# Optimization experiments

Measured on AMD Instinct MI355X. Metric: run time of the kernel, lower is better.

The kernel has to match this reference:

```python
import jax, jax.numpy as jnp
import numpy as np


def setup_inputs() -> dict:
    key = jax.random.key(0)
    k1, k2, k3 = jax.random.split(key, 3)
    B, T, D = 2, 2048, 1024
    x = jax.random.normal(k1, (B, T, D), dtype=jnp.float32)
    w_qkv = jax.random.normal(k2, (3 * D, D), dtype=jnp.float32) * (D ** -0.5)
    w_out = jax.random.normal(k3, (D, D), dtype=jnp.float32) * (D ** -0.5)
    return {"x": x, "w_qkv": w_qkv, "w_out": w_out, "heads": 16}


def reference(x, w_qkv, w_out, heads):
    # SelfAttention forward: attention_type='sdp', position_mode='alibi', causal=True, eval mode.
    B, T, D = x.shape
    H = heads
    hd = D // H
    scale = hd ** -0.5

    # qkv projection: torch Linear -> x @ W^T
    qkv = (x @ w_qkv.T).reshape(B, T, 3, H, hd)
    qkv = jnp.transpose(qkv, (2, 0, 3, 1, 4))  # [3, B, H, T, hd]
    q, k, v = qkv[0], qkv[1], qkv[2]

    # ALiBi relative bias: slopes = 1 / 2^(h/H) for h = 1..H
    slopes = 1.0 / jnp.power(2.0, jnp.arange(1, H + 1, dtype=jnp.float32) / H)
    pos = jnp.arange(T, dtype=jnp.float32)
    rel = jnp.abs(pos[:, None] - pos[None, :])  # [T, T]
    bias = -slopes[None, :, None, None] * rel[None, None, :, :]  # [1, H, T, T]

    # scores + causal mask + softmax (manual path since position_bias is not None)
    scores = jnp.einsum('bhqd,bhkd->bhqk', q, k) * scale + bias
    causal_mask = jnp.triu(jnp.ones((T, T), dtype=bool), k=1)
    scores = jnp.where(causal_mask[None, None, :, :], -jnp.inf, scores)
    attn = jax.nn.softmax(scores, axis=-1)
    attn = jnp.where(jnp.isnan(attn), 1.0 / float(max(T, 1)), attn)

    out = jnp.einsum('bhqk,bhkd->bhqd', attn, v)  # [B, H, T, hd]
    out = jnp.transpose(out, (0, 2, 1, 3)).reshape(B, T, D)
    return out @ w_out.T
```

## Files before the change

### kernel.cpp

```cpp
#include <hip/hip_runtime.h>
#include <hip/hip_bf16.h>

typedef __attribute__((ext_vector_type(8))) short shortx8;
typedef __attribute__((ext_vector_type(4))) float floatx4;
typedef __attribute__((ext_vector_type(16))) float floatx16;
typedef __attribute__((ext_vector_type(4))) unsigned uintx4;
typedef __attribute__((ext_vector_type(2))) unsigned uintx2;

#define B_ 2
#define T_ 2048
#define D_ 1024
#define H_ 16
#define HD_ 64
#define SCALE 0.125f
#define QSCALE 0.18033688011112042f
#define SMAX2 23.083120654223414f
#define FULLH ((size_t)B_ * H_ * T_ * HD_)

#define GLDS16(g, l) __builtin_amdgcn_global_load_lds( \
    (__attribute__((address_space(1))) void*)(g), \
    (__attribute__((address_space(3))) void*)(l), 16, 0, 0)

__device__ __forceinline__ short f2bf(float f) {
    union { float f; unsigned u; } v; v.f = f;
    unsigned r = v.u + 0x7FFFu + ((v.u >> 16) & 1u);
    return (short)(r >> 16);
}

__device__ __forceinline__ unsigned pk2(float x, float y) {
    union { __hip_bfloat162 h; unsigned u; } t;
    t.h = __float22bfloat162_rn(make_float2(x, y));
    return t.u;
}

__device__ __forceinline__ shortx8 cvt8(floatx4 a, floatx4 b) {
    uintx4 r = { pk2(a[0], a[1]), pk2(a[2], a[3]), pk2(b[0], b[1]), pk2(b[2], b[3]) };
    return __builtin_bit_cast(shortx8, r);
}

__device__ __forceinline__ float ex2(float x) {
#if __has_builtin(__builtin_amdgcn_exp2f)
    return __builtin_amdgcn_exp2f(x);
#else
    return exp2f(x);
#endif
}

__global__ __launch_bounds__(256) void cvt_xw(const float* __restrict__ x,
                                              const float* __restrict__ wqkv,
                                              short* __restrict__ xbf,
                                              short* __restrict__ wbf) {
    int i = blockIdx.x * 256 + threadIdx.x;
    const float* src; short* dst; int o;
    if (i < 524288) { src = x; dst = xbf; o = i; }
    else            { src = wqkv; dst = wbf; o = i - 524288; }
    const floatx4* p = reinterpret_cast<const floatx4*>(src) + (size_t)o * 2;
    *(reinterpret_cast<shortx8*>(dst) + o) = cvt8(p[0], p[1]);
}

__global__ __launch_bounds__(256) void qkv_fast(const short* __restrict__ xbf,
                                                const short* __restrict__ wbf,
                                                short* __restrict__ qout,
                                                short* __restrict__ kv) {
    __shared__ __align__(16) short As[128 * 64];
    __shared__ __align__(16) short Bs[128 * 64];

    const int tid = threadIdx.x;
    const int wv = tid >> 6;
    const int l  = tid & 63;
    const int ln = l & 15;
    const int quad = l >> 4;
    const int rowb = quad << 2;
    const int wm = wv >> 1, wn = wv & 1;

    const int id  = blockIdx.x;
    const int xcd = id & 7;
    const int tt  = id >> 3;
    const int bx  = xcd * 3 + (tt >> 5);
    const int by  = tt & 31;
    const int m0 = by * 128;
    const int n0g = bx * 128;

    const int lr = l >> 3, lc = l & 7;
    const int gcol = (lc ^ lr) << 3;
    const short* agp = xbf + (size_t)(m0 + wv * 32 + lr) * D_ + gcol;
    const short* bgp = wbf + (size_t)(n0g + wv * 32 + lr) * D_ + gcol;
    short* aldsb = As + wv * 32 * 64;
    short* bldsb = Bs + wv * 32 * 64;

    floatx4 acc[4][4] = {};

    for (int k0 = 0; k0 < D_; k0 += 64) {
        __syncthreads();
#pragma unroll
        for (int c = 0; c < 4; ++c) {
            GLDS16(agp + (size_t)(c * 8) * D_ + k0, aldsb + c * 512);
            GLDS16(bgp + (size_t)(c * 8) * D_ + k0, bldsb + c * 512);
        }
        __syncthreads();

#pragma unroll
        for (int kk = 0; kk < 2; ++kk) {
            const int csw = (kk << 2) + quad;
            const int sw = (csw ^ (ln & 7)) << 3;
            shortx8 af[4], bf[4];
#pragma unroll
            for (int i = 0; i < 4; ++i)
                af[i] = *reinterpret_cast<const shortx8*>(&As[((wm * 64 + i * 16 + ln) << 6) + sw]);
#pragma unroll
            for (int j = 0; j < 4; ++j)
                bf[j] = *reinterpret_cast<const shortx8*>(&Bs[((wn * 64 + j * 16 + ln) << 6) + sw]);
#pragma unroll
            for (int i = 0; i < 4; ++i)
#pragma unroll
                for (int j = 0; j < 4; ++j)
                    acc[i][j] = __builtin_amdgcn_mfma_f32_16x16x32_bf16(af[i], bf[j], acc[i][j], 0, 0, 0);
        }
    }

    const int sel = n0g >> 10;
    const int bb = m0 >> 11;
    const int t0w = (m0 + wm * 64) & (T_ - 1);
    const int h = ((n0g + wn * 64) >> 6) & 15;

    if (sel < 2) {
        short* dst = (sel == 0) ? qout : kv;
        const float sc = (sel == 0) ? QSCALE : 1.0f;
        const size_t hb = (size_t)(bb * H_ + h) * T_;
#pragma unroll
        for (int i = 0; i < 4; ++i)
#pragma unroll
            for (int r = 0; r < 4; ++r) {
                int t = t0w + i * 16 + rowb + r;
#pragma unroll
                for (int j = 0; j < 4; ++j)
                    dst[(hb + t) * HD_ + j * 16 + ln] = f2bf(acc[i][j][r] * sc);
            }
    } else {
        __syncthreads();
        short* tb = (wv < 2) ? (As + wv * 4096) : (Bs + (wv - 2) * 4096);
        short* vhead = kv + FULLH + (size_t)(bb * H_ + h) * HD_ * T_;
        const int dl = l & 31, th = (l >> 5) << 5;
#pragma unroll
        for (int p = 0; p < 2; ++p) {
#pragma unroll
            for (int i = 0; i < 4; ++i)
#pragma unroll
                for (int jj = 0; jj < 2; ++jj) {
                    int j = 2 * p + jj;
#pragma unroll
                    for (int r = 0; r < 4; ++r)
                        tb[(jj * 16 + ln) * 72 + i * 16 + rowb + r] = f2bf(acc[i][j][r]);
                }
            short* vd = vhead + (size_t)(p * 32 + dl) * T_ + t0w + th;
#pragma unroll
            for (int seg = 0; seg < 4; ++seg)
                *reinterpret_cast<shortx8*>(vd + seg * 8) =
                    *reinterpret_cast<const shortx8*>(&tb[dl * 72 + th + seg * 8]);
        }
    }
}

__global__ __launch_bounds__(256) void out_fast(const short* __restrict__ Abf,
                                                const short* __restrict__ wbf,
                                                float* __restrict__ out) {
    __shared__ __align__(16) short As[64 * 64];
    __shared__ __align__(16) short Bs[128 * 64];

    const int tid = threadIdx.x;
    const int wv = tid >> 6;
    const int l  = tid & 63;
    const int ln = l & 15;
    const int quad = l >> 4;
    const int rowb = quad << 2;
    const int wm = wv >> 1, wn = wv & 1;

    const int id = blockIdx.x;
    const int m0 = (id >> 3) * 64;
    const int n0g = (id & 7) * 128;

    const int lr = l >> 3, lc = l & 7;
    const int gcol = (lc ^ lr) << 3;
    const short* bgp = wbf + (size_t)(n0g + wv * 32 + lr) * D_ + gcol;
    short* aldsb = As + wv * 16 * 64;
    short* bldsb = Bs + wv * 32 * 64;

    size_t abase[2];
#pragma unroll
    for (int c = 0; c < 2; ++c) {
        int m = m0 + wv * 16 + c * 8 + lr;
        int bb2 = m >> 11, t = m & (T_ - 1);
        abase[c] = ((size_t)(bb2 * H_) * T_ + t) * HD_ + gcol;
    }

    floatx4 acc[2][4] = {};

    for (int k0 = 0; k0 < D_; k0 += 64) {
        const size_t hoff = (size_t)(k0 >> 6) * T_ * HD_;
        __syncthreads();
#pragma unroll
        for (int c = 0; c < 2; ++c)
            GLDS16(Abf + abase[c] + hoff, aldsb + c * 512);
#pragma unroll
        for (int c = 0; c < 4; ++c)
            GLDS16(bgp + (size_t)(c * 8) * D_ + k0, bldsb + c * 512);
        __syncthreads();

#pragma unroll
        for (int kk = 0; kk < 2; ++kk) {
            const int csw = (kk << 2) + quad;
            const int sw = (csw ^ (ln & 7)) << 3;
            shortx8 af[2], bf[4];
#pragma unroll
            for (int i = 0; i < 2; ++i)
                af[i] = *reinterpret_cast<const shortx8*>(&As[((wm * 32 + i * 16 + ln) << 6) + sw]);
#pragma unroll
            for (int j = 0; j < 4; ++j)
                bf[j] = *reinterpret_cast<const shortx8*>(&Bs[((wn * 64 + j * 16 + ln) << 6) + sw]);
#pragma unroll
            for (int i = 0; i < 2; ++i)
#pragma unroll
                for (int j = 0; j < 4; ++j)
                    acc[i][j] = __builtin_amdgcn_mfma_f32_16x16x32_bf16(af[i], bf[j], acc[i][j], 0, 0, 0);
        }
    }

#pragma unroll
    for (int i = 0; i < 2; ++i)
#pragma unroll
        for (int r = 0; r < 4; ++r) {
            int m = m0 + wm * 32 + i * 16 + rowb + r;
#pragma unroll
            for (int j = 0; j < 4; ++j)
                out[(size_t)m * D_ + n0g + wn * 64 + j * 16 + ln] = acc[i][j][r];
        }
}

__global__ __launch_bounds__(128, 2) void attn(const short* __restrict__ qws,
                                               const short* __restrict__ kv,
                                               short* ao,
                                               const float* __restrict__ wout,
                                               short* __restrict__ wobf) {
    if (blockIdx.x >= 1024) {
        int i = (blockIdx.x - 1024) * 128 + threadIdx.x;
        const floatx4* p = reinterpret_cast<const floatx4*>(wout) + (size_t)i * 2;
        *(reinterpret_cast<shortx8*>(wobf) + i) = cvt8(p[0], p[1]);
        return;
    }

    __shared__ __align__(16) short Ks[2][64][72];
    __shared__ __align__(16) short Vt[2][64][72];

    const int tid = threadIdx.x;
    const int wv = tid >> 6;
    const int l  = tid & 63;
    const int ql = l & 31;
    const int hi = l >> 5;

    const int id  = blockIdx.x;
    const int xcd = id & 7;
    const int u2  = (id >> 3) & 3;
    const int rr  = (id >> 5) & 7;
    const int tt  = id >> 8;
    const int bh  = xcd * 4 + u2;
    const int qblk = (tt == 0) ? 31 - rr : (tt == 1) ? rr : (tt == 2) ? 23 - rr : 8 + rr;
    const int h = bh & 15, b = bh >> 4;

    const float slope2 = 1.4426950408889634f * exp2f(-(float)(h + 1) * 0.0625f);
    const size_t koff = (size_t)(b * H_ + h) * T_ * HD_;
    const int q0w = qblk * 64 + wv * 32;
    const int e = qblk + 1;

    shortx8 qf[4];
#pragma unroll
    for (int ds = 0; ds < 4; ++ds)
        qf[ds] = *reinterpret_cast<const shortx8*>(&qws[koff + (size_t)(q0w + ql) * HD_ + ds * 16 + hi * 8]);

    const float cbase = slope2 * (float)(4 * hi - (q0w + ql)) - SMAX2;
    float rb[16];
#pragma unroll
    for (int g = 0; g < 16; ++g)
        rb[g] = cbase + slope2 * (float)((g & 3) + 8 * (g >> 2));
    const float s32 = slope2 * 32.0f;

    const int sr = tid >> 1;
    const int sc = (tid & 1) << 5;
    const short* kbase = kv + koff;
    const short* vbase = kv + FULLH + koff;
    shortx8 kR[4], vR[4];
    auto FETCH = [&](int kb) {
        const short* kp = kbase + (((size_t)(kb * 64 + sr)) << 6) + sc;
        const short* vp = vbase + (size_t)sr * T_ + kb * 64 + sc;
#pragma unroll
        for (int s = 0; s < 4; ++s) {
            kR[s] = *reinterpret_cast<const shortx8*>(kp + 8 * s);
            vR[s] = *reinterpret_cast<const shortx8*>(vp + 8 * s);
        }
    };
    auto STAGE = [&](int bi) {
#pragma unroll
        for (int s = 0; s < 4; ++s) {
            *reinterpret_cast<shortx8*>(&Ks[bi][sr][sc + 8 * s]) = kR[s];
            *reinterpret_cast<shortx8*>(&Vt[bi][sr][sc + 8 * s]) = vR[s];
        }
    };

    floatx16 o0 = {}, o1 = {}, ls = {};
    const shortx8 ones = {16256, 16256, 16256, 16256, 16256, 16256, 16256, 16256};
    const int qlh = ql - 4 * hi;

    FETCH(0);
    STAGE(0);
    if (e > 1) FETCH(1);
    __syncthreads();

    for (int kb = 0; kb < e; ++kb) {
        const int cur = kb & 1;
        if (kb + 1 < e) {
            STAGE(cur ^ 1);
            if (kb + 2 < e) FETCH(kb + 2);
        }

        const bool diag = (kb == qblk);
        const float tb = slope2 * (float)(kb * 64);

#pragma unroll
        for (int nc = 0; nc < 2; ++nc) {
            const bool act = !diag || (nc == 0) || (wv == 1);
            if (!act) continue;
            const bool part = diag && (nc == wv);

            floatx16 sacc = {};
#pragma unroll
            for (int ds = 0; ds < 4; ++ds) {
                shortx8 kf = *reinterpret_cast<const shortx8*>(&Ks[cur][nc * 32 + ql][ds * 16 + hi * 8]);
                sacc = __builtin_amdgcn_mfma_f32_32x32x16_bf16(kf, qf[ds], sacc, 0, 0, 0);
            }

            const float tnc = tb + (nc ? s32 : 0.0f);
            float p[16];
#pragma unroll
            for (int g = 0; g < 16; ++g) {
                float ev = ex2(sacc[g] + (rb[g] + tnc));
                if (part) {
                    const int kc2 = (g & 3) + 8 * (g >> 2);
                    ev = (kc2 <= qlh) ? ev : 0.0f;
                }
                p[g] = ev;
            }

            unsigned cv[4][2];
#pragma unroll
            for (int g = 0; g < 4; ++g) {
                cv[g][0] = pk2(p[4 * g + 0], p[4 * g + 1]);
                cv[g][1] = pk2(p[4 * g + 2], p[4 * g + 3]);
            }

            __builtin_amdgcn_s_setprio(1);
#pragma unroll
            for (int kh = 0; kh < 2; ++kh) {
                unsigned w0 = cv[2 * kh][0], w2 = cv[2 * kh + 1][0];
                unsigned w1 = cv[2 * kh][1], w3 = cv[2 * kh + 1][1];
                asm volatile("v_permlane32_swap_b32 %0, %1" : "+v"(w0), "+v"(w2));
                asm volatile("v_permlane32_swap_b32 %0, %1" : "+v"(w1), "+v"(w3));
                uintx4 uu = {w0, w1, w2, w3};
                shortx8 apv = __builtin_bit_cast(shortx8, uu);
                const int ks = nc * 2 + kh;
                ls = __builtin_amdgcn_mfma_f32_32x32x16_bf16(apv, ones, ls, 0, 0, 0);
                shortx8 vf0 = *reinterpret_cast<const shortx8*>(&Vt[cur][ql][ks * 16 + hi * 8]);
                o0 = __builtin_amdgcn_mfma_f32_32x32x16_bf16(apv, vf0, o0, 0, 0, 0);
                shortx8 vf1 = *reinterpret_cast<const shortx8*>(&Vt[cur][32 + ql][ks * 16 + hi * 8]);
                o1 = __builtin_amdgcn_mfma_f32_32x32x16_bf16(apv, vf1, o1, 0, 0, 0);
            }
            __builtin_amdgcn_s_setprio(0);
        }
        __syncthreads();
    }

#pragma unroll
    for (int g = 0; g < 16; ++g) {
        const int qrow = (g & 3) + 8 * (g >> 2) + 4 * hi;
        const float inv = 1.0f / ls[g];
        const size_t ob = koff + (size_t)(q0w + qrow) * HD_ + ql;
        ao[ob]      = f2bf(o0[g] * inv);
        ao[ob + 32] = f2bf(o1[g] * inv);
    }
}

__global__ __launch_bounds__(256) void qkv_slow(const float* __restrict__ x,
                                                const float* __restrict__ wqkv,
                                                short* __restrict__ qout,
                                                short* __restrict__ kv) {
    __shared__ __align__(16) short As[64][72];
    __shared__ __align__(16) short Bs[64][72];
    const int tid = threadIdx.x;
    const int wv = tid >> 6, l = tid & 63, ln = l & 15, quad = l >> 4, qd = quad << 3;
    const int m0 = blockIdx.y * 64;
    const int sel = blockIdx.x >> 4, h = blockIdx.x & 15;
    const int nrow = sel * D_ + h * HD_;
    const int sr0 = tid >> 3, sc0 = (tid & 7) << 3, sr1 = sr0 + 32;
    floatx4 fa[4], fb[4];
    auto FETCH = [&](int k0) {
        const float* ap = &x[(size_t)(m0 + sr0) * D_ + k0 + sc0];
        fa[0] = *reinterpret_cast<const floatx4*>(ap);
        fa[1] = *reinterpret_cast<const floatx4*>(ap + 4);
        ap += (size_t)32 * D_;
        fa[2] = *reinterpret_cast<const floatx4*>(ap);
        fa[3] = *reinterpret_cast<const floatx4*>(ap + 4);
        const float* bp = &wqkv[(size_t)(nrow + sr0) * D_ + k0 + sc0];
        fb[0] = *reinterpret_cast<const floatx4*>(bp);
        fb[1] = *reinterpret_cast<const floatx4*>(bp + 4);
        bp += (size_t)32 * D_;
        fb[2] = *reinterpret_cast<const floatx4*>(bp);
        fb[3] = *reinterpret_cast<const floatx4*>(bp + 4);
    };
    floatx4 acc[4] = {};
    FETCH(0);
    for (int k0 = 0; k0 < D_; k0 += 64) {
        __syncthreads();
        *reinterpret_cast<shortx8*>(&As[sr0][sc0]) = cvt8(fa[0], fa[1]);
        *reinterpret_cast<shortx8*>(&As[sr1][sc0]) = cvt8(fa[2], fa[3]);
        *reinterpret_cast<shortx8*>(&Bs[sr0][sc0]) = cvt8(fb[0], fb[1]);
        *reinterpret_cast<shortx8*>(&Bs[sr1][sc0]) = cvt8(fb[2], fb[3]);
        __syncthreads();
        if (k0 + 64 < D_) FETCH(k0 + 64);
        const int mr = (wv << 4) + ln;
#pragma unroll
        for (int kk = 0; kk < 2; ++kk) {
            shortx8 a = *reinterpret_cast<const shortx8*>(&As[mr][kk * 32 + qd]);
#pragma unroll
            for (int nc = 0; nc < 4; ++nc) {
                shortx8 bq = *reinterpret_cast<const shortx8*>(&Bs[nc * 16 + ln][kk * 32 + qd]);
                acc[nc] = __builtin_amdgcn_mfma_f32_16x16x32_bf16(a, bq, acc[nc], 0, 0, 0);
            }
        }
    }
    const int bb = m0 >> 11, t0 = m0 & (T_ - 1);
    if (sel < 2) {
        short* dst = (sel == 0) ? qout : kv;
        const float sc = (sel == 0) ? QSCALE : 1.0f;
#pragma unroll
        for (int r = 0; r < 4; ++r) {
            int t = t0 + (wv << 4) + (quad << 2) + r;
#pragma unroll
            for (int nc = 0; nc < 4; ++nc)
                dst[((size_t)(bb * H_ + h) * T_ + t) * HD_ + nc * 16 + ln] = f2bf(acc[nc][r] * sc);
        }
    } else {
        __syncthreads();
#pragma unroll
        for (int r = 0; r < 4; ++r)
#pragma unroll
            for (int nc = 0; nc < 4; ++nc)
                As[nc * 16 + ln][(wv << 4) + (quad << 2) + r] = f2bf(acc[nc][r]);
        __syncthreads();
        const int d = tid >> 2, tseg = (tid & 3) << 4;
        short* vdst = kv + FULLH + ((size_t)(bb * H_ + h) * HD_ + d) * T_ + t0 + tseg;
        *reinterpret_cast<shortx8*>(vdst)     = *reinterpret_cast<const shortx8*>(&As[d][tseg]);
        *reinterpret_cast<shortx8*>(vdst + 8) = *reinterpret_cast<const shortx8*>(&As[d][tseg + 8]);
    }
}

__global__ __launch_bounds__(256) void out_slow(const short* __restrict__ A,
                                                const float* __restrict__ W,
                                                float* __restrict__ out) {
    __shared__ __align__(16) short As[64][72];
    __shared__ __align__(16) short Bs[64][72];
    const int tid = threadIdx.x;
    const int wv = tid >> 6, l = tid & 63, ln = l & 15, quad = l >> 4, qd = quad << 3;
    const int m0 = blockIdx.y * 64, n0 = blockIdx.x * 64;
    const int sr0 = tid >> 3, sc0 = (tid & 7) << 3, sr1 = sr0 + 32;
    shortx8 sa0, sa1;
    floatx4 fb[4];
    auto FETCH = [&](int k0) {
        const int h = k0 >> 6;
        int m = m0 + sr0;
        int bb = m >> 11, t = m & (T_ - 1);
        sa0 = *reinterpret_cast<const shortx8*>(A + ((size_t)(bb * H_ + h) * T_ + t) * HD_ + sc0);
        m = m0 + sr1; bb = m >> 11; t = m & (T_ - 1);
        sa1 = *reinterpret_cast<const shortx8*>(A + ((size_t)(bb * H_ + h) * T_ + t) * HD_ + sc0);
        const float* bp = &W[(size_t)(n0 + sr0) * D_ + k0 + sc0];
        fb[0] = *reinterpret_cast<const floatx4*>(bp);
        fb[1] = *reinterpret_cast<const floatx4*>(bp + 4);
        bp += (size_t)32 * D_;
        fb[2] = *reinterpret_cast<const floatx4*>(bp);
        fb[3] = *reinterpret_cast<const floatx4*>(bp + 4);
    };
    floatx4 acc[4] = {};
    FETCH(0);
    for (int k0 = 0; k0 < D_; k0 += 64) {
        __syncthreads();
        *reinterpret_cast<shortx8*>(&As[sr0][sc0]) = sa0;
        *reinterpret_cast<shortx8*>(&As[sr1][sc0]) = sa1;
        *reinterpret_cast<shortx8*>(&Bs[sr0][sc0]) = cvt8(fb[0], fb[1]);
        *reinterpret_cast<shortx8*>(&Bs[sr1][sc0]) = cvt8(fb[2], fb[3]);
        __syncthreads();
        if (k0 + 64 < D_) FETCH(k0 + 64);
        const int mr = (wv << 4) + ln;
#pragma unroll
        for (int kk = 0; kk < 2; ++kk) {
            shortx8 a = *reinterpret_cast<const shortx8*>(&As[mr][kk * 32 + qd]);
#pragma unroll
            for (int nc = 0; nc < 4; ++nc) {
                shortx8 bq = *reinterpret_cast<const shortx8*>(&Bs[nc * 16 + ln][kk * 32 + qd]);
                acc[nc] = __builtin_amdgcn_mfma_f32_16x16x32_bf16(a, bq, acc[nc], 0, 0, 0);
            }
        }
    }
#pragma unroll
    for (int r = 0; r < 4; ++r) {
        int m = m0 + (wv << 4) + (quad << 2) + r;
#pragma unroll
        for (int nc = 0; nc < 4; ++nc)
            out[(size_t)m * D_ + n0 + nc * 16 + ln] = acc[nc][r];
    }
}

extern "C" void kernel_launch(void* const* d_in, const int* in_sizes, int n_in,
                              void* d_out, int out_size, void* d_ws, size_t ws_size,
                              hipStream_t stream) {
    const float* x    = (const float*)d_in[0];
    const float* wqkv = (const float*)d_in[1];
    const float* wout = (const float*)d_in[2];

    short* kvbuf = (short*)d_out;
    float* out   = (float*)d_out;

    if (ws_size >= 23068672ULL) {
        short* xbf  = (short*)d_ws;
        short* wbf  = xbf + 4 * 1024 * 1024;
        short* qws  = xbf + 7 * 1024 * 1024;
        short* wobf = xbf;

        cvt_xw<<<3584, 256, 0, stream>>>(x, wqkv, xbf, wbf);
        qkv_fast<<<dim3(768), 256, 0, stream>>>(xbf, wbf, qws, kvbuf);
        attn<<<dim3(2048), 128, 0, stream>>>(qws, kvbuf, qws, wout, wobf);
        out_fast<<<dim3(512), 256, 0, stream>>>(qws, wobf, out);
    } else {
        short* qws = (short*)d_ws;
        qkv_slow<<<dim3(48, 64), 256, 0, stream>>>(x, wqkv, qws, kvbuf);
        attn<<<dim3(1024), 128, 0, stream>>>(qws, kvbuf, qws, nullptr, nullptr);
        out_slow<<<dim3(16, 64), 256, 0, stream>>>(qws, wout, out);
    }
}
```

Before: 181.4 us.

## Double-buffer LDS tiles in QKV and output GEMMs and remap QKV block order

Both projection GEMMs now use two LDS buffers per operand. The next K-tile is prefetched with global_load_lds while the current tile feeds the MFMAs, which removes one barrier per iteration and hides global load latency. The QKV kernel also changes its block-to-tile mapping so that groups of 8 row tiles are walked per column group within each XCD, aiming for better L2 reuse. The cost is doubled LDS per block, which may lower occupancy, and the compiler may insert conservative waits that limit the overlap.

```diff
diff --git a/kernel.cpp b/kernel.cpp
--- a/kernel.cpp
+++ b/kernel.cpp
@@ -62,8 +62,8 @@
                                                 const short* __restrict__ wbf,
                                                 short* __restrict__ qout,
                                                 short* __restrict__ kv) {
-    __shared__ __align__(16) short As[128 * 64];
-    __shared__ __align__(16) short Bs[128 * 64];
+    __shared__ __align__(16) short As[2][128 * 64];
+    __shared__ __align__(16) short Bs[2][128 * 64];
 
     const int tid = threadIdx.x;
     const int wv = tid >> 6;
@@ -76,8 +76,12 @@
     const int id  = blockIdx.x;
     const int xcd = id & 7;
     const int tt  = id >> 3;
-    const int bx  = xcd * 3 + (tt >> 5);
-    const int by  = tt & 31;
+    const int byi = tt & 7;
+    const int u   = tt >> 3;
+    const int bxl = u % 3;
+    const int chunk = u / 3;
+    const int bx = xcd * 3 + bxl;
+    const int by = chunk * 8 + byi;
     const int m0 = by * 128;
     const int n0g = bx * 128;
 
@@ -85,19 +89,26 @@
     const int gcol = (lc ^ lr) << 3;
     const short* agp = xbf + (size_t)(m0 + wv * 32 + lr) * D_ + gcol;
     const short* bgp = wbf + (size_t)(n0g + wv * 32 + lr) * D_ + gcol;
-    short* aldsb = As + wv * 32 * 64;
-    short* bldsb = Bs + wv * 32 * 64;
 
     floatx4 acc[4][4] = {};
 
-    for (int k0 = 0; k0 < D_; k0 += 64) {
-        __syncthreads();
-#pragma unroll
-        for (int c = 0; c < 4; ++c) {
-            GLDS16(agp + (size_t)(c * 8) * D_ + k0, aldsb + c * 512);
-            GLDS16(bgp + (size_t)(c * 8) * D_ + k0, bldsb + c * 512);
-        }
-        __syncthreads();
+#pragma unroll
+    for (int c = 0; c < 4; ++c) {
+        GLDS16(agp + (size_t)(c * 8) * D_, &As[0][wv * 2048 + c * 512]);
+        GLDS16(bgp + (size_t)(c * 8) * D_, &Bs[0][wv * 2048 + c * 512]);
+    }
+
+    for (int it = 0; it < 16; ++it) {
+        const int cur = it & 1;
+        __syncthreads();
+        if (it < 15) {
+            const size_t k0n = (size_t)(it + 1) * 64;
+#pragma unroll
+            for (int c = 0; c < 4; ++c) {
+                GLDS16(agp + (size_t)(c * 8) * D_ + k0n, &As[cur ^ 1][wv * 2048 + c * 512]);
+                GLDS16(bgp + (size_t)(c * 8) * D_ + k0n, &Bs[cur ^ 1][wv * 2048 + c * 512]);
+            }
+        }
 
 #pragma unroll
         for (int kk = 0; kk < 2; ++kk) {
@@ -106,10 +117,10 @@
             shortx8 af[4], bf[4];
 #pragma unroll
             for (int i = 0; i < 4; ++i)
-                af[i] = *reinterpret_cast<const shortx8*>(&As[((wm * 64 + i * 16 + ln) << 6) + sw]);
+                af[i] = *reinterpret_cast<const shortx8*>(&As[cur][((wm * 64 + i * 16 + ln) << 6) + sw]);
 #pragma unroll
             for (int j = 0; j < 4; ++j)
-                bf[j] = *reinterpret_cast<const shortx8*>(&Bs[((wn * 64 + j * 16 + ln) << 6) + sw]);
+                bf[j] = *reinterpret_cast<const shortx8*>(&Bs[cur][((wn * 64 + j * 16 + ln) << 6) + sw]);
 #pragma unroll
             for (int i = 0; i < 4; ++i)
 #pragma unroll
@@ -138,7 +149,7 @@
             }
     } else {
         __syncthreads();
-        short* tb = (wv < 2) ? (As + wv * 4096) : (Bs + (wv - 2) * 4096);
+        short* tb = &As[0][0] + wv * 4096;
         short* vhead = kv + FULLH + (size_t)(bb * H_ + h) * HD_ * T_;
         const int dl = l & 31, th = (l >> 5) << 5;
 #pragma unroll
@@ -164,8 +175,8 @@
 __global__ __launch_bounds__(256) void out_fast(const short* __restrict__ Abf,
                                                 const short* __restrict__ wbf,
                                                 float* __restrict__ out) {
-    __shared__ __align__(16) short As[64 * 64];
-    __shared__ __align__(16) short Bs[128 * 64];
+    __shared__ __align__(16) short As[2][64 * 64];
+    __shared__ __align__(16) short Bs[2][128 * 64];
 
     const int tid = threadIdx.x;
     const int wv = tid >> 6;
@@ -182,8 +193,6 @@
     const int lr = l >> 3, lc = l & 7;
     const int gcol = (lc ^ lr) << 3;
     const short* bgp = wbf + (size_t)(n0g + wv * 32 + lr) * D_ + gcol;
-    short* aldsb = As + wv * 16 * 64;
-    short* bldsb = Bs + wv * 32 * 64;
 
     size_t abase[2];
 #pragma unroll
@@ -195,16 +204,26 @@
 
     floatx4 acc[2][4] = {};
 
-    for (int k0 = 0; k0 < D_; k0 += 64) {
-        const size_t hoff = (size_t)(k0 >> 6) * T_ * HD_;
-        __syncthreads();
-#pragma unroll
-        for (int c = 0; c < 2; ++c)
-            GLDS16(Abf + abase[c] + hoff, aldsb + c * 512);
-#pragma unroll
-        for (int c = 0; c < 4; ++c)
-            GLDS16(bgp + (size_t)(c * 8) * D_ + k0, bldsb + c * 512);
-        __syncthreads();
+#pragma unroll
+    for (int c = 0; c < 2; ++c)
+        GLDS16(Abf + abase[c], &As[0][wv * 1024 + c * 512]);
+#pragma unroll
+    for (int c = 0; c < 4; ++c)
+        GLDS16(bgp + (size_t)(c * 8) * D_, &Bs[0][wv * 2048 + c * 512]);
+
+    for (int it = 0; it < 16; ++it) {
+        const int cur = it & 1;
+        __syncthreads();
+        if (it < 15) {
+            const size_t hoffn = (size_t)(it + 1) * T_ * HD_;
+            const size_t k0n = (size_t)(it + 1) * 64;
+#pragma unroll
+            for (int c = 0; c < 2; ++c)
+                GLDS16(Abf + abase[c] + hoffn, &As[cur ^ 1][wv * 1024 + c * 512]);
+#pragma unroll
+            for (int c = 0; c < 4; ++c)
+                GLDS16(bgp + (size_t)(c * 8) * D_ + k0n, &Bs[cur ^ 1][wv * 2048 + c * 512]);
+        }
 
 #pragma unroll
         for (int kk = 0; kk < 2; ++kk) {
@@ -213,10 +232,10 @@
             shortx8 af[2], bf[4];
 #pragma unroll
             for (int i = 0; i < 2; ++i)
-                af[i] = *reinterpret_cast<const shortx8*>(&As[((wm * 32 + i * 16 + ln) << 6) + sw]);
+                af[i] = *reinterpret_cast<const shortx8*>(&As[cur][((wm * 32 + i * 16 + ln) << 6) + sw]);
 #pragma unroll
             for (int j = 0; j < 4; ++j)
-                bf[j] = *reinterpret_cast<const shortx8*>(&Bs[((wn * 64 + j * 16 + ln) << 6) + sw]);
+                bf[j] = *reinterpret_cast<const shortx8*>(&Bs[cur][((wn * 64 + j * 16 + ln) << 6) + sw]);
 #pragma unroll
             for (int i = 0; i < 2; ++i)
 #pragma unroll
```

Result: slower. 185.2 us (+2.1%).

## Fuse fp32-to-bf16 conversion into QKV GEMM with register-prefetched staging

Applied to the files above, without the earlier changes.

Removes the separate cvt_xw kernel and has the QKV GEMM load fp32 x and w_qkv directly, converting to bf16 in registers and writing padded LDS tiles. The next k-tile is prefetched into registers while MFMAs run, replacing the async global_load_lds path. This saves one launch and a bf16 round trip through global memory, but doubles the bytes each GEMM block reads from global memory and adds register pressure. The block-to-tile mapping is also reordered for L2 locality.

```diff
diff --git a/kernel.cpp b/kernel.cpp
--- a/kernel.cpp
+++ b/kernel.cpp
@@ -46,70 +46,73 @@
 #endif
 }
 
-__global__ __launch_bounds__(256) void cvt_xw(const float* __restrict__ x,
-                                              const float* __restrict__ wqkv,
-                                              short* __restrict__ xbf,
-                                              short* __restrict__ wbf) {
-    int i = blockIdx.x * 256 + threadIdx.x;
-    const float* src; short* dst; int o;
-    if (i < 524288) { src = x; dst = xbf; o = i; }
-    else            { src = wqkv; dst = wbf; o = i - 524288; }
-    const floatx4* p = reinterpret_cast<const floatx4*>(src) + (size_t)o * 2;
-    *(reinterpret_cast<shortx8*>(dst) + o) = cvt8(p[0], p[1]);
-}
-
-__global__ __launch_bounds__(256) void qkv_fast(const short* __restrict__ xbf,
-                                                const short* __restrict__ wbf,
+__global__ __launch_bounds__(256) void qkv_fast(const float* __restrict__ x,
+                                                const float* __restrict__ wqkv,
                                                 short* __restrict__ qout,
                                                 short* __restrict__ kv) {
-    __shared__ __align__(16) short As[128 * 64];
-    __shared__ __align__(16) short Bs[128 * 64];
+    __shared__ __align__(16) short As[128][72];
+    __shared__ __align__(16) short Bs[128][72];
 
     const int tid = threadIdx.x;
     const int wv = tid >> 6;
     const int l  = tid & 63;
     const int ln = l & 15;
     const int quad = l >> 4;
+    const int qd   = quad << 3;
     const int rowb = quad << 2;
     const int wm = wv >> 1, wn = wv & 1;
 
     const int id  = blockIdx.x;
     const int xcd = id & 7;
     const int tt  = id >> 3;
-    const int bx  = xcd * 3 + (tt >> 5);
-    const int by  = tt & 31;
+    const int byi = tt & 7;
+    const int u   = tt >> 3;
+    const int bxl = u % 3;
+    const int chunk = u / 3;
+    const int bx = xcd * 3 + bxl;
+    const int by = chunk * 8 + byi;
     const int m0 = by * 128;
     const int n0g = bx * 128;
 
-    const int lr = l >> 3, lc = l & 7;
-    const int gcol = (lc ^ lr) << 3;
-    const short* agp = xbf + (size_t)(m0 + wv * 32 + lr) * D_ + gcol;
-    const short* bgp = wbf + (size_t)(n0g + wv * 32 + lr) * D_ + gcol;
-    short* aldsb = As + wv * 32 * 64;
-    short* bldsb = Bs + wv * 32 * 64;
+    const int sr = tid >> 1;
+    const int sc = (tid & 1) << 5;
+    const float* agp = x    + (size_t)(m0 + sr) * D_ + sc;
+    const float* bgp = wqkv + (size_t)(n0g + sr) * D_ + sc;
+
+    floatx4 fa[8], fb[8];
+    auto FETCH = [&](int k0) {
+#pragma unroll
+        for (int s = 0; s < 8; ++s) {
+            fa[s] = *reinterpret_cast<const floatx4*>(agp + k0 + s * 4);
+            fb[s] = *reinterpret_cast<const floatx4*>(bgp + k0 + s * 4);
+        }
+    };
+    auto STAGE = [&]() {
+#pragma unroll
+        for (int s = 0; s < 4; ++s) {
+            *reinterpret_cast<shortx8*>(&As[sr][sc + 8 * s]) = cvt8(fa[2 * s], fa[2 * s + 1]);
+            *reinterpret_cast<shortx8*>(&Bs[sr][sc + 8 * s]) = cvt8(fb[2 * s], fb[2 * s + 1]);
+        }
+    };
 
     floatx4 acc[4][4] = {};
 
+    FETCH(0);
     for (int k0 = 0; k0 < D_; k0 += 64) {
         __syncthreads();
-#pragma unroll
-        for (int c = 0; c < 4; ++c) {
-            GLDS16(agp + (size_t)(c * 8) * D_ + k0, aldsb + c * 512);
-            GLDS16(bgp + (size_t)(c * 8) * D_ + k0, bldsb + c * 512);
-        }
-        __syncthreads();
+        STAGE();
+        __syncthreads();
+        if (k0 + 64 < D_) FETCH(k0 + 64);
 
 #pragma unroll
         for (int kk = 0; kk < 2; ++kk) {
-            const int csw = (kk << 2) + quad;
-            const int sw = (csw ^ (ln & 7)) << 3;
             shortx8 af[4], bf[4];
 #pragma unroll
             for (int i = 0; i < 4; ++i)
-                af[i] = *reinterpret_cast<const shortx8*>(&As[((wm * 64 + i * 16 + ln) << 6) + sw]);
+                af[i] = *reinterpret_cast<const shortx8*>(&As[wm * 64 + i * 16 + ln][kk * 32 + qd]);
 #pragma unroll
             for (int j = 0; j < 4; ++j)
-                bf[j] = *reinterpret_cast<const shortx8*>(&Bs[((wn * 64 + j * 16 + ln) << 6) + sw]);
+                bf[j] = *reinterpret_cast<const shortx8*>(&Bs[wn * 64 + j * 16 + ln][kk * 32 + qd]);
 #pragma unroll
             for (int i = 0; i < 4; ++i)
 #pragma unroll
@@ -125,7 +128,7 @@
 
     if (sel < 2) {
         short* dst = (sel == 0) ? qout : kv;
-        const float sc = (sel == 0) ? QSCALE : 1.0f;
+        const float sc2 = (sel == 0) ? QSCALE : 1.0f;
         const size_t hb = (size_t)(bb * H_ + h) * T_;
 #pragma unroll
         for (int i = 0; i < 4; ++i)
@@ -134,11 +137,11 @@
                 int t = t0w + i * 16 + rowb + r;
 #pragma unroll
                 for (int j = 0; j < 4; ++j)
-                    dst[(hb + t) * HD_ + j * 16 + ln] = f2bf(acc[i][j][r] * sc);
+                    dst[(hb + t) * HD_ + j * 16 + ln] = f2bf(acc[i][j][r] * sc2);
             }
     } else {
         __syncthreads();
-        short* tb = (wv < 2) ? (As + wv * 4096) : (Bs + (wv - 2) * 4096);
+        short* tb = &As[0][0] + wv * 2304;
         short* vhead = kv + FULLH + (size_t)(bb * H_ + h) * HD_ * T_;
         const int dl = l & 31, th = (l >> 5) << 5;
 #pragma unroll
@@ -527,13 +530,10 @@
     float* out   = (float*)d_out;
 
     if (ws_size >= 23068672ULL) {
-        short* xbf  = (short*)d_ws;
-        short* wbf  = xbf + 4 * 1024 * 1024;
-        short* qws  = xbf + 7 * 1024 * 1024;
-        short* wobf = xbf;
-
-        cvt_xw<<<3584, 256, 0, stream>>>(x, wqkv, xbf, wbf);
-        qkv_fast<<<dim3(768), 256, 0, stream>>>(xbf, wbf, qws, kvbuf);
+        short* qws  = (short*)d_ws;
+        short* wobf = qws + 4 * 1024 * 1024;
+
+        qkv_fast<<<dim3(768), 256, 0, stream>>>(x, wqkv, qws, kvbuf);
         attn<<<dim3(2048), 128, 0, stream>>>(qws, kvbuf, qws, wout, wobf);
         out_fast<<<dim3(512), 256, 0, stream>>>(qws, wobf, out);
     } else {
```

New measurement: 237.5 us. 31.0% more time.
